# Performance work log

Hardware: AMD Instinct MI355X
Metric: run time of the kernel (lower is better)

Reference implementation:

```python
import jax, jax.numpy as jnp
import numpy as np

C = 384       # channels
K = 20        # select_k
P = 96        # num_patches
B, N, H, W = 8, 16, 32, 32


def setup_inputs() -> dict:
    key = jax.random.key(0)
    k1, k2, k3 = jax.random.split(key, 3)
    feature = jax.random.normal(k1, (B, N, C, H, W), dtype=jnp.float32)
    dw_w = jax.random.normal(k2, (C, 1, 3, 3), dtype=jnp.float32) * 0.05  # depthwise kernel (OIHW, groups=C)
    dw_b = jnp.zeros((C,), dtype=jnp.float32)
    pw_w = jax.random.normal(k3, (1, C, 1, 1), dtype=jnp.float32) * 0.05  # pointwise kernel
    pw_b = jnp.zeros((1,), dtype=jnp.float32)
    return {"feature": feature, "dw_w": dw_w, "dw_b": dw_b, "pw_w": pw_w, "pw_b": pw_b}


def reference(feature, dw_w, dw_b, pw_w, pw_b):
    b, n, c, h, w = feature.shape
    bn = b * n
    x = feature.reshape(bn, c, h, w)
    # depthwise 3x3 conv (groups = c)
    x = jax.lax.conv_general_dilated(
        x, dw_w, window_strides=(1, 1), padding='SAME',
        feature_group_count=c, dimension_numbers=('NCHW', 'OIHW', 'NCHW')
    ) + dw_b[None, :, None, None]
    # pointwise 1x1 conv -> 1 channel
    x = jax.lax.conv_general_dilated(
        x, pw_w, window_strides=(1, 1), padding='SAME',
        dimension_numbers=('NCHW', 'OIHW', 'NCHW')
    ) + pw_b[None, :, None, None]
    score = jax.nn.sigmoid(x).reshape(bn, h * w)

    # top-k voted patches (descending, sorted -> matches torch.topk)
    vote_values, vote_indices = jax.lax.top_k(score, K)

    # boolean scatter mask of selected positions
    mask = jnp.zeros((bn, h * w), dtype=bool)
    mask = mask.at[jnp.arange(bn)[:, None], vote_indices].set(True)

    # unselected indices in ascending order per row (stable sort: False first)
    unselected = jnp.argsort(mask, axis=1, stable=True)[:, : h * w - K]

    # single random permutation shared across rows (torch.randperm + expand)
    num_remaining = P - K
    perm = jax.random.permutation(jax.random.key(42), h * w - K)[:num_remaining]
    random_remaining = unselected[:, perm]

    x_coords = vote_indices % w
    y_coords = vote_indices // w
    # NOTE: original module keeps only the first n rows of the b*n batch
    x_select = jnp.clip(x_coords[:n, :], 1, w - 1)
    y_select = jnp.clip(y_coords[:n, :], 1, h - 1)
    x_remain = jnp.clip((random_remaining % w)[:n, :], 1, w - 1)
    y_remain = jnp.clip((random_remaining // w)[:n, :], 1, h - 1)

    x_out = jnp.concatenate([x_select, x_remain], axis=1)  # [n, P]
    y_out = jnp.concatenate([y_select, y_remain], axis=1)  # [n, P]
    return (x_out, y_out)
```

## Files before the change

kernel.cpp:

```cpp
#include <hip/hip_runtime.h>
#include <cstdint>
#include <cstddef>
#include <algorithm>

#define NROW 16
#define CTOT 384
#define HW   1024
#define KSEL 20
#define PSEL 96
#define NREM 76
#define NUNSEL 1004

#define CPB   8
#define SPLIT (CTOT / CPB)

typedef unsigned long long u64;

struct Perm76 { int p[NREM]; };

__device__ __forceinline__ void conv_job(const float4* f6, const float* w9,
                                         int b, int c, float acc[4][4])
{
  #pragma unroll
  for (int m = 0; m < 6; ++m) {
    float4 f = f6[m];
    const bool dead = (b == 0 && m == 0) || (b == 7 && m == 5);
    if (dead) { f.x = 0.f; f.y = 0.f; f.z = 0.f; f.w = 0.f; }
    float L = __shfl_up(f.w, 1);
    float R = __shfl_down(f.x, 1);
    if (c == 0) L = 0.f;
    if (c == 7) R = 0.f;
    const float c6[6] = { L, f.x, f.y, f.z, f.w, R };
    #pragma unroll
    for (int j = 0; j < 4; ++j) {
      const int d = m - j;
      if (d >= 0 && d < 3) {
        #pragma unroll
        for (int k = 0; k < 4; ++k)
          acc[j][k] += c6[k]     * w9[3 * d]
                     + c6[k + 1] * w9[3 * d + 1]
                     + c6[k + 2] * w9[3 * d + 2];
      }
    }
  }
}

__global__ __launch_bounds__(256) void pv_conv(
    const float* __restrict__ feat, const float* __restrict__ dw_w,
    const float* __restrict__ pw_w, float* __restrict__ partial,
    int* __restrict__ ticket)
{
  __shared__ float red[4][HW];
  const int t = threadIdx.x;
  const int w = t >> 6, lane = t & 63;
  const int b = lane >> 3, c = lane & 7;
  const int r = blockIdx.x & (NROW - 1);
  const int s = blockIdx.x >> 4;

  if (s == 0 && t == 0) ticket[r] = 0;

  const int chA = s * CPB + 2 * w;
  const float* baseA = feat + ((size_t)r * CTOT + chA) * HW;
  const float* baseB = baseA + HW;

  float4 fa[6], fb[6];
  #pragma unroll
  for (int m = 0; m < 6; ++m) {
    const int row = 4 * b + m - 1;
    const int rc = row < 0 ? 0 : (row > 31 ? 31 : row);
    fa[m] = *reinterpret_cast<const float4*>(baseA + rc * 32 + 4 * c);
  }
  #pragma unroll
  for (int m = 0; m < 6; ++m) {
    const int row = 4 * b + m - 1;
    const int rc = row < 0 ? 0 : (row > 31 ? 31 : row);
    fb[m] = *reinterpret_cast<const float4*>(baseB + rc * 32 + 4 * c);
  }

  float wA[9], wB[9];
  {
    const float pa = pw_w[chA], pb = pw_w[chA + 1];
    #pragma unroll
    for (int i = 0; i < 9; ++i) {
      wA[i] = dw_w[chA * 9 + i] * pa;
      wB[i] = dw_w[(chA + 1) * 9 + i] * pb;
    }
  }

  float acc[4][4];
  #pragma unroll
  for (int j = 0; j < 4; ++j)
    #pragma unroll
    for (int k = 0; k < 4; ++k) acc[j][k] = 0.f;

  conv_job(fa, wA, b, c, acc);
  conv_job(fb, wB, b, c, acc);

  #pragma unroll
  for (int j = 0; j < 4; ++j)
    *reinterpret_cast<float4*>(&red[w][(4 * b + j) * 32 + 4 * c]) =
        make_float4(acc[j][0], acc[j][1], acc[j][2], acc[j][3]);
  __syncthreads();

  float4 sum = make_float4(0.f, 0.f, 0.f, 0.f);
  #pragma unroll
  for (int g = 0; g < 4; ++g) {
    const float4 v = *reinterpret_cast<const float4*>(&red[g][4 * t]);
    sum.x += v.x; sum.y += v.y; sum.z += v.z; sum.w += v.w;
  }
  *reinterpret_cast<float4*>(partial + ((size_t)(r * SPLIT + s)) * HW + 4 * t) = sum;
}

__global__ __launch_bounds__(256) void pv_reduceSelect(
    const float* __restrict__ partial, u64* __restrict__ cand,
    int* __restrict__ ticket, int* __restrict__ out, Perm76 perm)
{
  __shared__ float red[8][128];
  __shared__ u64 keysh[128];
  __shared__ u64 candL[8 * KSEL];
  __shared__ int votes[KSEL];
  __shared__ int maskv[HW];
  __shared__ int wsumS[4];
  __shared__ int unsel[NUNSEL];
  __shared__ int isFinS;

  const int r = blockIdx.x >> 3;
  const int q = blockIdx.x & 7;
  const int t = threadIdx.x;
  const int sg = t >> 5, l32 = t & 31;

  const float* bp = partial + ((size_t)(r * SPLIT + sg)) * HW + q * 128 + 4 * l32;
  float4 a = make_float4(0.f, 0.f, 0.f, 0.f);
  #pragma unroll
  for (int i = 0; i < 6; ++i) {
    const float4 v = *reinterpret_cast<const float4*>(bp + (size_t)(8 * i) * HW);
    a.x += v.x; a.y += v.y; a.z += v.z; a.w += v.w;
  }
  *reinterpret_cast<float4*>(&red[sg][4 * l32]) = a;
  __syncthreads();

  if (t < 128) {
    float sc = 0.f;
    #pragma unroll
    for (int g = 0; g < 8; ++g) sc += red[g][t];
    const uint32_t bb = __float_as_uint(sc);
    const uint32_t mm = (bb & 0x80000000u) ? ~bb : (bb | 0x80000000u);
    const int gpx = q * 128 + t;
    keysh[t] = ((u64)mm << 32) | (uint32_t)(1023 - gpx);
  }
  __syncthreads();
  if (t < 128) {
    const u64 my = keysh[t];
    int rank = 0;
    for (int j = 0; j < 128; ++j) rank += (keysh[j] > my);
    if (rank < KSEL)
      atomicExch(&cand[((size_t)(r * 8 + q)) * KSEL + rank], my);
  }
  __syncthreads();

  if (t == 0) isFinS = (atomicAdd(&ticket[r], 1) == 7);
  __syncthreads();
  if (!isFinS) return;

  if (t < 8 * KSEL) candL[t] = atomicAdd(&cand[(size_t)r * 8 * KSEL + t], 0ull);
  maskv[t] = 0; maskv[t + 256] = 0; maskv[t + 512] = 0; maskv[t + 768] = 0;
  __syncthreads();

  if (t < 8 * KSEL) {
    const u64 my = candL[t];
    int rank = 0;
    for (int j = 0; j < 8 * KSEL; ++j) rank += (candL[j] > my);
    if (rank < KSEL) votes[rank] = 1023 - (int)(my & 1023ull);
  }
  __syncthreads();

  if (t < KSEL) {
    const int idx = votes[t];
    maskv[idx] = 1;
    int xx = idx & 31, yy = idx >> 5;
    if (xx < 1) xx = 1;
    if (yy < 1) yy = 1;
    out[r * PSEL + t]               = xx;
    out[NROW * PSEL + r * PSEL + t] = yy;
  }
  __syncthreads();

  const int lane = t & 63, wv = t >> 6;
  int cnt = 0;
  #pragma unroll
  for (int j = 0; j < 4; ++j) cnt += (maskv[t * 4 + j] == 0);
  int inc = cnt;
  #pragma unroll
  for (int dd = 1; dd < 64; dd <<= 1) {
    const int o = __shfl_up(inc, dd);
    if (lane >= dd) inc += o;
  }
  if (lane == 63) wsumS[wv] = inc;
  __syncthreads();
  int basep = 0;
  for (int i = 0; i < 4; ++i) if (i < wv) basep += wsumS[i];
  int pos = basep + inc - cnt;
  #pragma unroll
  for (int j = 0; j < 4; ++j) {
    const int i = t * 4 + j;
    if (!maskv[i]) unsel[pos++] = i;
  }
  __syncthreads();

  if (t < NREM) {
    const int u = unsel[perm.p[t]];
    int xx = u & 31, yy = u >> 5;
    if (xx < 1) xx = 1;
    if (yy < 1) yy = 1;
    out[r * PSEL + KSEL + t]               = xx;
    out[NROW * PSEL + r * PSEL + KSEL + t] = yy;
  }
}

static inline uint32_t rotl32(uint32_t v, uint32_t n) { return (v << n) | (v >> (32 - n)); }

static void tf2x32(uint32_t k0, uint32_t k1, uint32_t x0, uint32_t x1,
                   uint32_t* o0, uint32_t* o1)
{
  const uint32_t ks[3] = { k0, k1, k0 ^ k1 ^ 0x1BD11BDAu };
  static const uint32_t rot[2][4] = { {13, 15, 26, 6}, {17, 29, 16, 24} };
  x0 += ks[0]; x1 += ks[1];
  for (int i = 0; i < 5; ++i) {
    const uint32_t* rr = rot[i & 1];
    for (int j = 0; j < 4; ++j) { x0 += x1; x1 = rotl32(x1, rr[j]); x1 ^= x0; }
    x0 += ks[(i + 1) % 3];
    x1 += ks[(i + 2) % 3] + (uint32_t)(i + 1);
  }
  *o0 = x0; *o1 = x1;
}

static void compute_perm(int* perm_out)
{
  uint32_t bits[NUNSEL];
  uint32_t sk0, sk1;
  { uint32_t o0, o1; tf2x32(0u, 42u, 0u, 1u, &o0, &o1); sk0 = o0; sk1 = o1; }
  for (int i = 0; i < NUNSEL; ++i) {
    uint32_t o0, o1; tf2x32(sk0, sk1, 0u, (uint32_t)i, &o0, &o1);
    bits[i] = o0 ^ o1;
  }
  int idx[NUNSEL];
  for (int i = 0; i < NUNSEL; ++i) idx[i] = i;
  std::stable_sort(idx, idx + NUNSEL, [&](int a, int b) { return bits[a] < bits[b]; });
  for (int j = 0; j < NREM; ++j) perm_out[j] = idx[j];
}

extern "C" void kernel_launch(void* const* d_in, const int* in_sizes, int n_in,
                              void* d_out, int out_size, void* d_ws, size_t ws_size,
                              hipStream_t stream)
{
  (void)in_sizes; (void)n_in; (void)out_size; (void)ws_size;
  const float* feat = (const float*)d_in[0];
  const float* dw_w = (const float*)d_in[1];
  const float* pw_w = (const float*)d_in[3];
  int*   out     = (int*)d_out;
  float* partial = (float*)d_ws;
  u64*   cand    = (u64*)((char*)d_ws + (size_t)NROW * SPLIT * HW * sizeof(float));
  int*   ticket  = (int*)(cand + (size_t)NROW * 8 * KSEL);

  Perm76 perm;
  compute_perm(perm.p);

  pv_conv<<<NROW * SPLIT, 256, 0, stream>>>(feat, dw_w, pw_w, partial, ticket);
  pv_reduceSelect<<<128, 256, 0, stream>>>(partial, cand, ticket, out, perm);
}
```

Measured before the change: 18.05 us.

## Restructure depthwise conv to one channel per half-wave with 8-row tiles

Each half-wavefront now handles one full channel, each lane computing an 8x4 output tile. Halo rows and columns come from cross-lane shuffles within the half-wave, where the old code reloaded six rows per four outputs from memory for two channels per wave. This cuts redundant global loads from vertical halo overlap. The cost is more registers, more shuffles, and a larger padded shared buffer (8 planes of 1040 floats) for the cross-channel reduction, which may lower occupancy.

```diff
diff --git a/kernel.cpp b/kernel.cpp
--- a/kernel.cpp
+++ b/kernel.cpp
@@ -13,102 +13,113 @@
 
 #define CPB   8
 #define SPLIT (CTOT / CPB)
+#define PLW   1040
 
 typedef unsigned long long u64;
 
 struct Perm76 { int p[NREM]; };
-
-__device__ __forceinline__ void conv_job(const float4* f6, const float* w9,
-                                         int b, int c, float acc[4][4])
-{
-  #pragma unroll
-  for (int m = 0; m < 6; ++m) {
-    float4 f = f6[m];
-    const bool dead = (b == 0 && m == 0) || (b == 7 && m == 5);
-    if (dead) { f.x = 0.f; f.y = 0.f; f.z = 0.f; f.w = 0.f; }
-    float L = __shfl_up(f.w, 1);
-    float R = __shfl_down(f.x, 1);
-    if (c == 0) L = 0.f;
-    if (c == 7) R = 0.f;
-    const float c6[6] = { L, f.x, f.y, f.z, f.w, R };
-    #pragma unroll
-    for (int j = 0; j < 4; ++j) {
-      const int d = m - j;
-      if (d >= 0 && d < 3) {
-        #pragma unroll
-        for (int k = 0; k < 4; ++k)
-          acc[j][k] += c6[k]     * w9[3 * d]
-                     + c6[k + 1] * w9[3 * d + 1]
-                     + c6[k + 2] * w9[3 * d + 2];
-      }
-    }
-  }
-}
 
 __global__ __launch_bounds__(256) void pv_conv(
     const float* __restrict__ feat, const float* __restrict__ dw_w,
     const float* __restrict__ pw_w, float* __restrict__ partial,
     int* __restrict__ ticket)
 {
-  __shared__ float red[4][HW];
+  __shared__ float red[8 * PLW];
   const int t = threadIdx.x;
   const int w = t >> 6, lane = t & 63;
-  const int b = lane >> 3, c = lane & 7;
+  const int h = lane & 31, hb = lane & 32;
+  const int b = h >> 3, c = h & 7;
   const int r = blockIdx.x & (NROW - 1);
   const int s = blockIdx.x >> 4;
 
   if (s == 0 && t == 0) ticket[r] = 0;
 
-  const int chA = s * CPB + 2 * w;
-  const float* baseA = feat + ((size_t)r * CTOT + chA) * HW;
-  const float* baseB = baseA + HW;
-
-  float4 fa[6], fb[6];
-  #pragma unroll
-  for (int m = 0; m < 6; ++m) {
-    const int row = 4 * b + m - 1;
-    const int rc = row < 0 ? 0 : (row > 31 ? 31 : row);
-    fa[m] = *reinterpret_cast<const float4*>(baseA + rc * 32 + 4 * c);
-  }
-  #pragma unroll
-  for (int m = 0; m < 6; ++m) {
-    const int row = 4 * b + m - 1;
-    const int rc = row < 0 ? 0 : (row > 31 ? 31 : row);
-    fb[m] = *reinterpret_cast<const float4*>(baseB + rc * 32 + 4 * c);
-  }
-
-  float wA[9], wB[9];
+  const int ch = s * CPB + 2 * w + (lane >> 5);
+  const float* base = feat + ((size_t)r * CTOT + ch) * HW + 4 * c;
+
+  float4 f[8];
+  #pragma unroll
+  for (int j = 0; j < 8; ++j)
+    f[j] = *reinterpret_cast<const float4*>(base + (8 * b + j) * 32);
+
+  float w9[9];
   {
-    const float pa = pw_w[chA], pb = pw_w[chA + 1];
-    #pragma unroll
-    for (int i = 0; i < 9; ++i) {
-      wA[i] = dw_w[chA * 9 + i] * pa;
-      wB[i] = dw_w[(chA + 1) * 9 + i] * pb;
+    const float pw = pw_w[ch];
+    #pragma unroll
+    for (int i = 0; i < 9; ++i) w9[i] = dw_w[ch * 9 + i] * pw;
+  }
+
+  const int sm = hb | ((h - 8) & 31), sp = hb | ((h + 8) & 31);
+  float4 fm, fp;
+  fm.x = __shfl(f[7].x, sm); fm.y = __shfl(f[7].y, sm);
+  fm.z = __shfl(f[7].z, sm); fm.w = __shfl(f[7].w, sm);
+  fp.x = __shfl(f[0].x, sp); fp.y = __shfl(f[0].y, sp);
+  fp.z = __shfl(f[0].z, sp); fp.w = __shfl(f[0].w, sp);
+  if (b == 0) { fm.x = 0.f; fm.y = 0.f; fm.z = 0.f; fm.w = 0.f; }
+  if (b == 3) { fp.x = 0.f; fp.y = 0.f; fp.z = 0.f; fp.w = 0.f; }
+
+  float L[10], R[10];
+  #pragma unroll
+  for (int k = 1; k <= 8; ++k) {
+    L[k] = __shfl(f[k - 1].w, hb | ((h - 1) & 31));
+    R[k] = __shfl(f[k - 1].x, hb | ((h + 1) & 31));
+  }
+  L[0] = __shfl(f[7].w, hb | ((h - 9) & 31));
+  R[0] = __shfl(f[7].x, hb | ((h - 7) & 31));
+  L[9] = __shfl(f[0].w, hb | ((h + 7) & 31));
+  R[9] = __shfl(f[0].x, hb | ((h + 9) & 31));
+  if (b == 0) { L[0] = 0.f; R[0] = 0.f; }
+  if (b == 3) { L[9] = 0.f; R[9] = 0.f; }
+  if (c == 0) {
+    #pragma unroll
+    for (int k = 0; k < 10; ++k) L[k] = 0.f;
+  }
+  if (c == 7) {
+    #pragma unroll
+    for (int k = 0; k < 10; ++k) R[k] = 0.f;
+  }
+
+  float acc[8][4];
+  #pragma unroll
+  for (int j = 0; j < 8; ++j)
+    #pragma unroll
+    for (int k = 0; k < 4; ++k) acc[j][k] = 0.f;
+
+  #pragma unroll
+  for (int j = 0; j < 8; ++j) {
+    #pragma unroll
+    for (int d = 0; d < 3; ++d) {
+      const int k = j + d;
+      const float4 C = (k == 0) ? fm : (k == 9 ? fp : f[k - 1]);
+      const float a0 = L[k], a1 = C.x, a2 = C.y, a3 = C.z, a4 = C.w, a5 = R[k];
+      const float t0 = w9[3 * d], t1 = w9[3 * d + 1], t2 = w9[3 * d + 2];
+      acc[j][0] += a0 * t0 + a1 * t1 + a2 * t2;
+      acc[j][1] += a1 * t0 + a2 * t1 + a3 * t2;
+      acc[j][2] += a2 * t0 + a3 * t1 + a4 * t2;
+      acc[j][3] += a3 * t0 + a4 * t1 + a5 * t2;
     }
   }
 
-  float acc[4][4];
-  #pragma unroll
-  for (int j = 0; j < 4; ++j)
-    #pragma unroll
-    for (int k = 0; k < 4; ++k) acc[j][k] = 0.f;
-
-  conv_job(fa, wA, b, c, acc);
-  conv_job(fb, wB, b, c, acc);
-
-  #pragma unroll
-  for (int j = 0; j < 4; ++j)
-    *reinterpret_cast<float4*>(&red[w][(4 * b + j) * 32 + 4 * c]) =
-        make_float4(acc[j][0], acc[j][1], acc[j][2], acc[j][3]);
-  __syncthreads();
-
-  float4 sum = make_float4(0.f, 0.f, 0.f, 0.f);
-  #pragma unroll
-  for (int g = 0; g < 4; ++g) {
-    const float4 v = *reinterpret_cast<const float4*>(&red[g][4 * t]);
-    sum.x += v.x; sum.y += v.y; sum.z += v.z; sum.w += v.w;
-  }
-  *reinterpret_cast<float4*>(partial + ((size_t)(r * SPLIT + s)) * HW + 4 * t) = sum;
+  {
+    float* pl = &red[(2 * w + (lane >> 5)) * PLW + b * 260 + 4 * c];
+    #pragma unroll
+    for (int j = 0; j < 8; ++j)
+      *reinterpret_cast<float4*>(pl + j * 32) =
+          make_float4(acc[j][0], acc[j][1], acc[j][2], acc[j][3]);
+  }
+  __syncthreads();
+
+  {
+    const int row = t >> 3;
+    const int off = (row >> 3) * 260 + (row & 7) * 32 + 4 * (t & 7);
+    float4 sum = make_float4(0.f, 0.f, 0.f, 0.f);
+    #pragma unroll
+    for (int p = 0; p < 8; ++p) {
+      const float4 v = *reinterpret_cast<const float4*>(&red[p * PLW + off]);
+      sum.x += v.x; sum.y += v.y; sum.z += v.z; sum.w += v.w;
+    }
+    *reinterpret_cast<float4*>(partial + ((size_t)(r * SPLIT + s)) * HW + 4 * t) = sum;
+  }
 }
 
 __global__ __launch_bounds__(256) void pv_reduceSelect(
```

After: 17.60 us, median of 2. -2.5%, faster.
